# Kernel optimization log

Hardware: AMD Instinct MI355X
Metric: run time of the kernel (lower is better)

## Reference

```python
import jax, jax.numpy as jnp
import numpy as np

B, D, H, C = 131072, 256, 256, 8
TAU = 0.15


def setup_inputs() -> dict:
    key = jax.random.key(0)
    ks = jax.random.split(key, 10)
    s_in = 1.0 / np.sqrt(D)
    s_h = 1.0 / np.sqrt(H)
    return {
        "x": jax.random.normal(ks[0], (B, D), jnp.float32),
        # root node params
        "W1": jax.random.normal(ks[1], (D, H), jnp.float32) * s_in,
        "b1": jnp.zeros((H,), jnp.float32),
        "W2": jax.random.normal(ks[2], (H, C), jnp.float32) * s_h,
        "b2": jnp.zeros((C,), jnp.float32),
        # one leaf child per class: stacked params [C, ...]
        "Wc1": jax.random.normal(ks[3], (C, H, H), jnp.float32) * s_h,
        "bc1": jnp.zeros((C, H), jnp.float32),
        "Wc2": jax.random.normal(ks[4], (C, H, C), jnp.float32) * s_h,
        "bc2": jnp.zeros((C, C), jnp.float32),
        "tau": jnp.full((C,), TAU, jnp.float32),
    }


def reference(x, W1, b1, W2, b2, Wc1, bc1, Wc2, bc2, tau):
    # root dense + head
    h = jax.nn.relu(x @ W1 + b1)            # [B, H]
    logits = h @ W2 + b2                    # [B, C]
    probs = jax.nn.softmax(logits, axis=1)  # [B, C]

    # route(): walk classes in descending prob order, take the first class
    # that has a child (all C do here) and whose prob >= tau[class].
    # Equivalent vectorized form: argmax of probs restricted to passing classes.
    mask = probs >= tau                     # [B, C]
    routed = jnp.any(mask, axis=1)          # [B]
    masked = jnp.where(mask, probs, -1.0)
    best = jnp.argmax(masked, axis=1)       # [B] chosen child per sample

    out_logits, out_h = logits, h
    for c in range(C):                      # small fixed expert loop
        sel = (routed & (best == c))[:, None]
        h_c = jax.nn.relu(h @ Wc1[c] + bc1[c])  # [B, H]
        l_c = h_c @ Wc2[c] + bc2[c]             # [B, C]
        out_logits = jnp.where(sel, l_c, out_logits)
        out_h = jnp.where(sel, h_c, out_h)

    depths = routed.astype(jnp.int32)       # leaf children => depth 1, else 0
    return out_logits, out_h, depths
```

## Files before the change

kernel.cpp:

```cpp
#include <hip/hip_runtime.h>

#define Bn 131072
#define Dn 256
#define Hn 256
#define Cn 8

typedef __attribute__((ext_vector_type(4))) float f32x4;
typedef __attribute__((ext_vector_type(8))) __bf16 bf16x8;
typedef _Float16 f16;
typedef __attribute__((ext_vector_type(8))) _Float16 f16x8;

#define LDA 40

__device__ inline unsigned short rtn_bf16(float v) {
    unsigned int u = __float_as_uint(v);
    unsigned int r = u + 0x7fffu + ((u >> 16) & 1u);
    return (unsigned short)(r >> 16);
}
__device__ inline float bf16_to_f(unsigned short h) {
    return __uint_as_float((unsigned int)h << 16);
}
__device__ inline ushort4 cvt4(float4 v) {
    return make_ushort4(rtn_bf16(v.x), rtn_bf16(v.y), rtn_bf16(v.z), rtn_bf16(v.w));
}
__device__ inline void split2h(float v, unsigned short& a0, unsigned short& a1) {
    const f16 h0 = (f16)v;
    const f16 h1 = (f16)(v - (float)h0);
    a0 = __builtin_bit_cast(unsigned short, h0);
    a1 = __builtin_bit_cast(unsigned short, h1);
}

__global__ __launch_bounds__(256)
void prep_kernel(const float* __restrict__ W1, const float* __restrict__ Wc1,
                 unsigned short* __restrict__ W1t0, unsigned short* __restrict__ W1t1,
                 unsigned short* __restrict__ Wc1t)
{
    const int idx = blockIdx.x * 256 + threadIdx.x;
    if (idx < 65536) {
        const int n = idx >> 8, k = idx & 255;
        unsigned short a0, a1;
        split2h(W1[k * 256 + n], a0, a1);
        W1t0[idx] = a0; W1t1[idx] = a1;
    } else {
        const int j = idx - 65536;
        const int e = j >> 16, rem = j & 65535;
        const int n = rem >> 8, k = rem & 255;
        Wc1t[(e << 16) + n * 256 + k] = rtn_bf16(Wc1[(e << 16) + k * 256 + n]);
    }
}

__global__ __launch_bounds__(512, 4)
void root_kernel(const float* __restrict__ x,
                 const unsigned short* __restrict__ Wt0,
                 const unsigned short* __restrict__ Wt1,
                 const float* __restrict__ b1, const float* __restrict__ W2,
                 const float* __restrict__ b2, const float* __restrict__ tau,
                 float* __restrict__ out_logits, float* __restrict__ out_h,
                 float* __restrict__ out_depth, int* __restrict__ cnt,
                 int* __restrict__ lists)
{
    __shared__ unsigned short sA0[128 * LDA], sA1[128 * LDA];
    __shared__ float sP[128][8];
    __shared__ int   sCnt[8], sBase[8], sBest[128], sSlot[128];

    const int t    = threadIdx.x;
    const int lane = t & 63;
    const int w    = t >> 6;
    const int tx   = lane & 15;
    const int q    = lane >> 4;
    const long r0  = (long)blockIdx.x * 128;

    if (t < 8) sCnt[t] = 0;
    ((float*)sP)[t] = 0.0f;
    ((float*)sP)[t + 512] = 0.0f;

    const int colA = w * 32 + tx;
    const int colB = colA + 16;
    const unsigned short* bp0 = Wt0 + colA * 256 + q * 8;
    const unsigned short* bp1 = Wt1 + colA * 256 + q * 8;
    const unsigned short* bp2 = Wt0 + colB * 256 + q * 8;
    const unsigned short* bp3 = Wt1 + colB * 256 + q * 8;

    f32x4 acc[8][2];
#pragma unroll
    for (int mt = 0; mt < 8; mt++)
#pragma unroll
        for (int nt = 0; nt < 2; nt++) acc[mt][nt] = (f32x4)0.0f;

    const int ar = t >> 3, ak = t & 7;
    const float4* xr0 = (const float4*)x + (r0 + ar) * 64 + ak;
    const float4* xr1 = (const float4*)x + (r0 + 64 + ar) * 64 + ak;
    float4 xv0 = xr0[0];
    float4 xv1 = xr1[0];

    for (int i = 0; i < 8; i++) {
        if (i) __syncthreads();
        {
            unsigned short h0[4], h1[4];
            split2h(xv0.x, h0[0], h1[0]);
            split2h(xv0.y, h0[1], h1[1]);
            split2h(xv0.z, h0[2], h1[2]);
            split2h(xv0.w, h0[3], h1[3]);
            *(ushort4*)&sA0[ar * LDA + ak * 4] = make_ushort4(h0[0], h0[1], h0[2], h0[3]);
            *(ushort4*)&sA1[ar * LDA + ak * 4] = make_ushort4(h1[0], h1[1], h1[2], h1[3]);
            split2h(xv1.x, h0[0], h1[0]);
            split2h(xv1.y, h0[1], h1[1]);
            split2h(xv1.z, h0[2], h1[2]);
            split2h(xv1.w, h0[3], h1[3]);
            *(ushort4*)&sA0[(64 + ar) * LDA + ak * 4] = make_ushort4(h0[0], h0[1], h0[2], h0[3]);
            *(ushort4*)&sA1[(64 + ar) * LDA + ak * 4] = make_ushort4(h1[0], h1[1], h1[2], h1[3]);
        }
        if (i < 7) { xv0 = xr0[(i + 1) * 8]; xv1 = xr1[(i + 1) * 8]; }
        __syncthreads();

        const int ko = i * 32;
        const f16x8 B0 = *(const f16x8*)(bp0 + ko);
        const f16x8 B1 = *(const f16x8*)(bp1 + ko);
        const f16x8 B2 = *(const f16x8*)(bp2 + ko);
        const f16x8 B3 = *(const f16x8*)(bp3 + ko);

#pragma unroll
        for (int mt = 0; mt < 8; mt++) {
            const f16x8 A0 = *(const f16x8*)&sA0[(mt * 16 + tx) * LDA + q * 8];
            const f16x8 A1 = *(const f16x8*)&sA1[(mt * 16 + tx) * LDA + q * 8];
            acc[mt][0] = __builtin_amdgcn_mfma_f32_16x16x32_f16(A0, B0, acc[mt][0], 0, 0, 0);
            acc[mt][0] = __builtin_amdgcn_mfma_f32_16x16x32_f16(A0, B1, acc[mt][0], 0, 0, 0);
            acc[mt][0] = __builtin_amdgcn_mfma_f32_16x16x32_f16(A1, B0, acc[mt][0], 0, 0, 0);
            acc[mt][1] = __builtin_amdgcn_mfma_f32_16x16x32_f16(A0, B2, acc[mt][1], 0, 0, 0);
            acc[mt][1] = __builtin_amdgcn_mfma_f32_16x16x32_f16(A0, B3, acc[mt][1], 0, 0, 0);
            acc[mt][1] = __builtin_amdgcn_mfma_f32_16x16x32_f16(A1, B2, acc[mt][1], 0, 0, 0);
        }
    }

    const float b1c0 = b1[colA], b1c1 = b1[colB];
    float w20[8], w21[8];
    {
        const float4 a0 = ((const float4*)W2)[colA * 2];
        const float4 a1 = ((const float4*)W2)[colA * 2 + 1];
        const float4 c0 = ((const float4*)W2)[colB * 2];
        const float4 c1 = ((const float4*)W2)[colB * 2 + 1];
        w20[0]=a0.x; w20[1]=a0.y; w20[2]=a0.z; w20[3]=a0.w;
        w20[4]=a1.x; w20[5]=a1.y; w20[6]=a1.z; w20[7]=a1.w;
        w21[0]=c0.x; w21[1]=c0.y; w21[2]=c0.z; w21[3]=c0.w;
        w21[4]=c1.x; w21[5]=c1.y; w21[6]=c1.z; w21[7]=c1.w;
    }

#pragma unroll
    for (int mt = 0; mt < 8; mt++) {
        float pm[4][8];
#pragma unroll
        for (int reg = 0; reg < 4; reg++) {
            const float h0 = fmaxf(acc[mt][0][reg] + b1c0, 0.0f);
            const float h1 = fmaxf(acc[mt][1][reg] + b1c1, 0.0f);
            const int row = mt * 16 + q * 4 + reg;
            out_h[(r0 + row) * 256 + colA] = h0;
            out_h[(r0 + row) * 256 + colB] = h1;
#pragma unroll
            for (int c = 0; c < 8; c++)
                pm[reg][c] = h0 * w20[c] + h1 * w21[c];
        }
#pragma unroll
        for (int reg = 0; reg < 4; reg++)
#pragma unroll
            for (int c = 0; c < 8; c++) {
                float v = pm[reg][c];
                v += __shfl_xor(v, 1, 16);
                v += __shfl_xor(v, 2, 16);
                v += __shfl_xor(v, 4, 16);
                v += __shfl_xor(v, 8, 16);
                if (tx == 0) atomicAdd(&sP[mt * 16 + q * 4 + reg][c], v);
            }
    }
    __syncthreads();

    if (t < 128) {
        const long row = r0 + t;
        float l[8];
        float mx = -1e30f;
#pragma unroll
        for (int c = 0; c < 8; c++) {
            l[c] = sP[t][c] + b2[c];
            mx = fmaxf(mx, l[c]);
        }
        float e[8], s = 0.0f;
#pragma unroll
        for (int c = 0; c < 8; c++) { e[c] = expf(l[c] - mx); s += e[c]; }
        const float inv = 1.0f / s;
        int best = 0; float bp = -1.0f;
#pragma unroll
        for (int c = 0; c < 8; c++) {
            const float pr = e[c] * inv;
            const float m  = (pr >= tau[c]) ? pr : -1.0f;
            if (m > bp) { bp = m; best = c; }
        }
        const bool routed = (bp >= 0.0f);
        float4* lo4 = (float4*)&out_logits[row * 8];
        lo4[0] = make_float4(l[0], l[1], l[2], l[3]);
        lo4[1] = make_float4(l[4], l[5], l[6], l[7]);
        out_depth[row] = routed ? 1.0f : 0.0f;
        if (routed) {
            sSlot[t] = atomicAdd(&sCnt[best], 1);
            sBest[t] = best;
        } else {
            sBest[t] = -1;
        }
    }
    __syncthreads();
    if (t < 8) sBase[t] = sCnt[t] ? atomicAdd(&cnt[t], sCnt[t]) : 0;
    __syncthreads();
    if (t < 128 && sBest[t] >= 0) {
        const int e = sBest[t];
        lists[(long)e * Bn + sBase[e] + sSlot[t]] = (int)(r0 + t);
    }
}

__global__ __launch_bounds__(512, 4)
void expert_kernel(const unsigned short* __restrict__ Wc1t,
                   const float* __restrict__ bc1,
                   const float* __restrict__ Wc2, const float* __restrict__ bc2,
                   float* __restrict__ out_logits, float* __restrict__ out_h,
                   const int* __restrict__ cnt, const int* __restrict__ lists)
{
    const int e = blockIdx.y;
    const int n = cnt[e];
    const int tile0 = blockIdx.x * 128;
    if (tile0 >= n) return;
    const int nrows = min(128, n - tile0);

    __shared__ unsigned short sA[2][128 * LDA];
    __shared__ float sP[128][8];
    __shared__ int   sRidx[128];

    const int t    = threadIdx.x;
    const int lane = t & 63;
    const int w    = t >> 6;
    const int tx   = lane & 15;
    const int q    = lane >> 4;

    if (t < 128) sRidx[t] = lists[(long)e * Bn + tile0 + min(t, nrows - 1)];
    ((float*)sP)[t] = 0.0f;
    ((float*)sP)[t + 512] = 0.0f;

    const unsigned short* W = Wc1t + (long)e * 65536;
    const int colA = w * 32 + tx;
    const int colB = colA + 16;
    const unsigned short* bpA = W + colA * 256 + q * 8;
    const unsigned short* bpB = W + colB * 256 + q * 8;

    f32x4 acc[8][2];
#pragma unroll
    for (int mt = 0; mt < 8; mt++)
#pragma unroll
        for (int nt = 0; nt < 2; nt++) acc[mt][nt] = (f32x4)0.0f;

    const int ar = t >> 3, ak = t & 7;
    __syncthreads();
    const float4* hr0 = (const float4*)out_h + (long)sRidx[ar] * 64 + ak;
    const float4* hr1 = (const float4*)out_h + (long)sRidx[64 + ar] * 64 + ak;

    float4 xv0 = hr0[0], xv1 = hr1[0];
    *(ushort4*)&sA[0][ar * LDA + ak * 4]        = cvt4(xv0);
    *(ushort4*)&sA[0][(64 + ar) * LDA + ak * 4] = cvt4(xv1);
    xv0 = hr0[8]; xv1 = hr1[8];
    bf16x8 BcA = *(const bf16x8*)(bpA);
    bf16x8 BcB = *(const bf16x8*)(bpB);
    __syncthreads();

#pragma unroll 2
    for (int i = 0; i < 8; i++) {
        const int cur = i & 1;
        if (i < 7) {
            *(ushort4*)&sA[cur ^ 1][ar * LDA + ak * 4]        = cvt4(xv0);
            *(ushort4*)&sA[cur ^ 1][(64 + ar) * LDA + ak * 4] = cvt4(xv1);
            if (i < 6) { xv0 = hr0[(i + 2) * 8]; xv1 = hr1[(i + 2) * 8]; }
        }
        bf16x8 BnA, BnB;
        if (i < 7) {
            BnA = *(const bf16x8*)(bpA + (i + 1) * 32);
            BnB = *(const bf16x8*)(bpB + (i + 1) * 32);
        }
#pragma unroll
        for (int mt = 0; mt < 8; mt++) {
            const bf16x8 A = *(const bf16x8*)&sA[cur][(mt * 16 + tx) * LDA + q * 8];
            acc[mt][0] = __builtin_amdgcn_mfma_f32_16x16x32_bf16(A, BcA, acc[mt][0], 0, 0, 0);
            acc[mt][1] = __builtin_amdgcn_mfma_f32_16x16x32_bf16(A, BcB, acc[mt][1], 0, 0, 0);
        }
        if (i < 7) { BcA = BnA; BcB = BnB; }
        __syncthreads();
    }

    const float* bc1e = bc1 + (long)e * Hn;
    const float b1c0 = bc1e[colA], b1c1 = bc1e[colB];
    const float* W2c = Wc2 + (long)e * Hn * Cn;
    float w20[8], w21[8];
    {
        const float4 a0 = ((const float4*)W2c)[colA * 2];
        const float4 a1 = ((const float4*)W2c)[colA * 2 + 1];
        const float4 c0 = ((const float4*)W2c)[colB * 2];
        const float4 c1 = ((const float4*)W2c)[colB * 2 + 1];
        w20[0]=a0.x; w20[1]=a0.y; w20[2]=a0.z; w20[3]=a0.w;
        w20[4]=a1.x; w20[5]=a1.y; w20[6]=a1.z; w20[7]=a1.w;
        w21[0]=c0.x; w21[1]=c0.y; w21[2]=c0.z; w21[3]=c0.w;
        w21[4]=c1.x; w21[5]=c1.y; w21[6]=c1.z; w21[7]=c1.w;
    }

#pragma unroll
    for (int mt = 0; mt < 8; mt++) {
        float pm[4][8];
#pragma unroll
        for (int reg = 0; reg < 4; reg++) {
            const float h0 = fmaxf(acc[mt][0][reg] + b1c0, 0.0f);
            const float h1 = fmaxf(acc[mt][1][reg] + b1c1, 0.0f);
            const int row = mt * 16 + q * 4 + reg;
            if (row < nrows) {
                out_h[(long)sRidx[row] * 256 + colA] = h0;
                out_h[(long)sRidx[row] * 256 + colB] = h1;
            }
#pragma unroll
            for (int c = 0; c < 8; c++)
                pm[reg][c] = h0 * w20[c] + h1 * w21[c];
        }
#pragma unroll
        for (int reg = 0; reg < 4; reg++)
#pragma unroll
            for (int c = 0; c < 8; c++) {
                float v = pm[reg][c];
                v += __shfl_xor(v, 1, 16);
                v += __shfl_xor(v, 2, 16);
                v += __shfl_xor(v, 4, 16);
                v += __shfl_xor(v, 8, 16);
                if (tx == 0) atomicAdd(&sP[mt * 16 + q * 4 + reg][c], v);
            }
    }
    __syncthreads();

    if (t < nrows) {
        const long row = sRidx[t];
        const float* bc2e = bc2 + (long)e * Cn;
        float4* lo4 = (float4*)&out_logits[row * 8];
        lo4[0] = make_float4(sP[t][0] + bc2e[0], sP[t][1] + bc2e[1],
                             sP[t][2] + bc2e[2], sP[t][3] + bc2e[3]);
        lo4[1] = make_float4(sP[t][4] + bc2e[4], sP[t][5] + bc2e[5],
                             sP[t][6] + bc2e[6], sP[t][7] + bc2e[7]);
    }
}

extern "C" void kernel_launch(void* const* d_in, const int* in_sizes, int n_in,
                              void* d_out, int out_size, void* d_ws, size_t ws_size,
                              hipStream_t stream)
{
    const float* x   = (const float*)d_in[0];
    const float* W1  = (const float*)d_in[1];
    const float* b1  = (const float*)d_in[2];
    const float* W2  = (const float*)d_in[3];
    const float* b2  = (const float*)d_in[4];
    const float* Wc1 = (const float*)d_in[5];
    const float* bc1 = (const float*)d_in[6];
    const float* Wc2 = (const float*)d_in[7];
    const float* bc2 = (const float*)d_in[8];
    const float* tau = (const float*)d_in[9];

    float* out_logits = (float*)d_out;
    float* out_h      = out_logits + (long)Bn * Cn;
    float* out_depth  = out_h + (long)Bn * Hn;

    char* wsb = (char*)d_ws;
    int* cnt   = (int*)wsb;
    int* lists = (int*)(wsb + 128);
    unsigned short* W1t0 = (unsigned short*)(wsb + 128 + (size_t)8 * Bn * 4);
    unsigned short* W1t1 = W1t0 + 65536;
    unsigned short* Wc1t = W1t1 + 65536;

    hipMemsetAsync(d_ws, 0, 128, stream);

    prep_kernel<<<dim3((65536 + 8 * 65536) / 256), 256, 0, stream>>>(
        W1, Wc1, W1t0, W1t1, Wc1t);

    root_kernel<<<dim3(Bn / 128), 512, 0, stream>>>(
        x, W1t0, W1t1, b1, W2, b2, tau, out_logits, out_h, out_depth,
        cnt, lists);

    expert_kernel<<<dim3(Bn / 128, 8), 512, 0, stream>>>(
        Wc1t, bc1, Wc2, bc2, out_logits, out_h, cnt, lists);
}
```

Before: 599.9 us.

## Stage root hidden activations as bf16 scratch and halve expert tile rows

The root kernel now writes h as bf16 into a workspace buffer and stores fp32 h to the output only for unrouted rows. This cuts the fp32 out_h write for routed rows and the fp32 reload in the expert kernel. The expert kernel gathers bf16 rows directly and uses 64-row tiles instead of 128, which doubles the number of blocks and improves load balance and occupancy across uneven expert counts. The new path depends on the workspace being large enough to hold the buffer and falls back to the old path otherwise.

```diff
diff --git a/kernel.cpp b/kernel.cpp
--- a/kernel.cpp
+++ b/kernel.cpp
@@ -49,6 +49,7 @@
     }
 }
 
+template <int HB>
 __global__ __launch_bounds__(512, 4)
 void root_kernel(const float* __restrict__ x,
                  const unsigned short* __restrict__ Wt0,
@@ -57,7 +58,7 @@
                  const float* __restrict__ b2, const float* __restrict__ tau,
                  float* __restrict__ out_logits, float* __restrict__ out_h,
                  float* __restrict__ out_depth, int* __restrict__ cnt,
-                 int* __restrict__ lists)
+                 int* __restrict__ lists, unsigned short* __restrict__ hbuf)
 {
     __shared__ unsigned short sA0[128 * LDA], sA1[128 * LDA];
     __shared__ float sP[128][8];
@@ -153,8 +154,13 @@
             const float h0 = fmaxf(acc[mt][0][reg] + b1c0, 0.0f);
             const float h1 = fmaxf(acc[mt][1][reg] + b1c1, 0.0f);
             const int row = mt * 16 + q * 4 + reg;
-            out_h[(r0 + row) * 256 + colA] = h0;
-            out_h[(r0 + row) * 256 + colB] = h1;
+            if (HB) {
+                hbuf[(r0 + row) * 256 + colA] = rtn_bf16(h0);
+                hbuf[(r0 + row) * 256 + colB] = rtn_bf16(h1);
+            } else {
+                out_h[(r0 + row) * 256 + colA] = h0;
+                out_h[(r0 + row) * 256 + colB] = h1;
+            }
 #pragma unroll
             for (int c = 0; c < 8; c++)
                 pm[reg][c] = h0 * w20[c] + h1 * w21[c];
@@ -207,6 +213,18 @@
     }
     __syncthreads();
     if (t < 8) sBase[t] = sCnt[t] ? atomicAdd(&cnt[t], sCnt[t]) : 0;
+    if (HB) {
+#pragma unroll
+        for (int mt = 0; mt < 8; mt++)
+#pragma unroll
+            for (int reg = 0; reg < 4; reg++) {
+                const int row = mt * 16 + q * 4 + reg;
+                if (sBest[row] < 0) {
+                    out_h[(r0 + row) * 256 + colA] = fmaxf(acc[mt][0][reg] + b1c0, 0.0f);
+                    out_h[(r0 + row) * 256 + colB] = fmaxf(acc[mt][1][reg] + b1c1, 0.0f);
+                }
+            }
+    }
     __syncthreads();
     if (t < 128 && sBest[t] >= 0) {
         const int e = sBest[t];
@@ -214,22 +232,24 @@
     }
 }
 
+template <int HB>
 __global__ __launch_bounds__(512, 4)
 void expert_kernel(const unsigned short* __restrict__ Wc1t,
                    const float* __restrict__ bc1,
                    const float* __restrict__ Wc2, const float* __restrict__ bc2,
                    float* __restrict__ out_logits, float* __restrict__ out_h,
-                   const int* __restrict__ cnt, const int* __restrict__ lists)
+                   const int* __restrict__ cnt, const int* __restrict__ lists,
+                   const unsigned short* __restrict__ hbuf)
 {
     const int e = blockIdx.y;
     const int n = cnt[e];
-    const int tile0 = blockIdx.x * 128;
+    const int tile0 = blockIdx.x * 64;
     if (tile0 >= n) return;
-    const int nrows = min(128, n - tile0);
-
-    __shared__ unsigned short sA[2][128 * LDA];
-    __shared__ float sP[128][8];
-    __shared__ int   sRidx[128];
+    const int nrows = min(64, n - tile0);
+
+    __shared__ unsigned short sA[2][64 * LDA];
+    __shared__ float sP[64][8];
+    __shared__ int   sRidx[64];
 
     const int t    = threadIdx.x;
     const int lane = t & 63;
@@ -237,9 +257,8 @@
     const int tx   = lane & 15;
     const int q    = lane >> 4;
 
-    if (t < 128) sRidx[t] = lists[(long)e * Bn + tile0 + min(t, nrows - 1)];
+    if (t < 64) sRidx[t] = lists[(long)e * Bn + tile0 + min(t, nrows - 1)];
     ((float*)sP)[t] = 0.0f;
-    ((float*)sP)[t + 512] = 0.0f;
 
     const unsigned short* W = Wc1t + (long)e * 65536;
     const int colA = w * 32 + tx;
@@ -247,21 +266,24 @@
     const unsigned short* bpA = W + colA * 256 + q * 8;
     const unsigned short* bpB = W + colB * 256 + q * 8;
 
-    f32x4 acc[8][2];
-#pragma unroll
-    for (int mt = 0; mt < 8; mt++)
+    f32x4 acc[4][2];
+#pragma unroll
+    for (int mt = 0; mt < 4; mt++)
 #pragma unroll
         for (int nt = 0; nt < 2; nt++) acc[mt][nt] = (f32x4)0.0f;
 
     const int ar = t >> 3, ak = t & 7;
     __syncthreads();
-    const float4* hr0 = (const float4*)out_h + (long)sRidx[ar] * 64 + ak;
-    const float4* hr1 = (const float4*)out_h + (long)sRidx[64 + ar] * 64 + ak;
-
-    float4 xv0 = hr0[0], xv1 = hr1[0];
-    *(ushort4*)&sA[0][ar * LDA + ak * 4]        = cvt4(xv0);
-    *(ushort4*)&sA[0][(64 + ar) * LDA + ak * 4] = cvt4(xv1);
-    xv0 = hr0[8]; xv1 = hr1[8];
+
+    const unsigned short* hrB = hbuf + (long)sRidx[ar] * 256 + ak * 4;
+    const float4*         hrF = (const float4*)out_h + (long)sRidx[ar] * 64 + ak;
+
+    ushort4 xv;
+    if (HB) xv = *(const ushort4*)(hrB);
+    else    xv = cvt4(hrF[0]);
+    *(ushort4*)&sA[0][ar * LDA + ak * 4] = xv;
+    if (HB) xv = *(const ushort4*)(hrB + 32);
+    else    xv = cvt4(hrF[8]);
     bf16x8 BcA = *(const bf16x8*)(bpA);
     bf16x8 BcB = *(const bf16x8*)(bpB);
     __syncthreads();
@@ -270,9 +292,11 @@
     for (int i = 0; i < 8; i++) {
         const int cur = i & 1;
         if (i < 7) {
-            *(ushort4*)&sA[cur ^ 1][ar * LDA + ak * 4]        = cvt4(xv0);
-            *(ushort4*)&sA[cur ^ 1][(64 + ar) * LDA + ak * 4] = cvt4(xv1);
-            if (i < 6) { xv0 = hr0[(i + 2) * 8]; xv1 = hr1[(i + 2) * 8]; }
+            *(ushort4*)&sA[cur ^ 1][ar * LDA + ak * 4] = xv;
+            if (i < 6) {
+                if (HB) xv = *(const ushort4*)(hrB + (i + 2) * 32);
+                else    xv = cvt4(hrF[(i + 2) * 8]);
+            }
         }
         bf16x8 BnA, BnB;
         if (i < 7) {
@@ -280,7 +304,7 @@
             BnB = *(const bf16x8*)(bpB + (i + 1) * 32);
         }
 #pragma unroll
-        for (int mt = 0; mt < 8; mt++) {
+        for (int mt = 0; mt < 4; mt++) {
             const bf16x8 A = *(const bf16x8*)&sA[cur][(mt * 16 + tx) * LDA + q * 8];
             acc[mt][0] = __builtin_amdgcn_mfma_f32_16x16x32_bf16(A, BcA, acc[mt][0], 0, 0, 0);
             acc[mt][1] = __builtin_amdgcn_mfma_f32_16x16x32_bf16(A, BcB, acc[mt][1], 0, 0, 0);
@@ -305,7 +329,7 @@
     }
 
 #pragma unroll
-    for (int mt = 0; mt < 8; mt++) {
+    for (int mt = 0; mt < 4; mt++) {
         float pm[4][8];
 #pragma unroll
         for (int reg = 0; reg < 4; reg++) {
@@ -370,16 +394,27 @@
     unsigned short* W1t0 = (unsigned short*)(wsb + 128 + (size_t)8 * Bn * 4);
     unsigned short* W1t1 = W1t0 + 65536;
     unsigned short* Wc1t = W1t1 + 65536;
+    unsigned short* hbuf = Wc1t + 8 * 65536;
+
+    const size_t need_hbuf = (size_t)((char*)(hbuf + (size_t)Bn * 256) - wsb);
+    const bool   use_hbuf  = ws_size >= need_hbuf;
 
     hipMemsetAsync(d_ws, 0, 128, stream);
 
     prep_kernel<<<dim3((65536 + 8 * 65536) / 256), 256, 0, stream>>>(
         W1, Wc1, W1t0, W1t1, Wc1t);
 
-    root_kernel<<<dim3(Bn / 128), 512, 0, stream>>>(
-        x, W1t0, W1t1, b1, W2, b2, tau, out_logits, out_h, out_depth,
-        cnt, lists);
-
-    expert_kernel<<<dim3(Bn / 128, 8), 512, 0, stream>>>(
-        Wc1t, bc1, Wc2, bc2, out_logits, out_h, cnt, lists);
-}
+    if (use_hbuf) {
+        root_kernel<1><<<dim3(Bn / 128), 512, 0, stream>>>(
+            x, W1t0, W1t1, b1, W2, b2, tau, out_logits, out_h, out_depth,
+            cnt, lists, hbuf);
+        expert_kernel<1><<<dim3(Bn / 64, 8), 512, 0, stream>>>(
+            Wc1t, bc1, Wc2, bc2, out_logits, out_h, cnt, lists, hbuf);
+    } else {
+        root_kernel<0><<<dim3(Bn / 128), 512, 0, stream>>>(
+            x, W1t0, W1t1, b1, W2, b2, tau, out_logits, out_h, out_depth,
+            cnt, lists, hbuf);
+        expert_kernel<0><<<dim3(Bn / 64, 8), 512, 0, stream>>>(
+            Wc1t, bc1, Wc2, bc2, out_logits, out_h, cnt, lists, hbuf);
+    }
+}
```

Result: faster. 564.2 us (-6.0%).
